# Kernel tuning notes

Hardware: AMD Instinct MI355X
Metric: run time of the kernel (lower is better)

Reference implementation:

```python
import jax, jax.numpy as jnp
import numpy as np

NUM_CONCAT = 3

def setup_inputs() -> dict:
    key = jax.random.key(0)
    k1, k2, k3 = jax.random.split(key, 3)
    x = jax.random.normal(k1, (4, 2048, 4096), dtype=jnp.float32)
    W = jax.random.normal(k2, (12288, 4096), dtype=jnp.float32) * 0.02
    b = jax.random.normal(k3, (12288,), dtype=jnp.float32) * 0.02
    return {"x": x, "W": W, "b": b}

def reference(x, W, b):
    # Fused concat-linear: one GEMM over the concatenated weight, then split.
    # x: [B, S, D]; W: [NUM_CONCAT*H, D]; b: [NUM_CONCAT*H]
    y = jnp.einsum('bsd,od->bso', x, W) + b  # [B, S, NUM_CONCAT*H]
    hidden = y.shape[-1] // NUM_CONCAT
    return tuple(y[..., i * hidden:(i + 1) * hidden] for i in range(NUM_CONCAT))
```

## Files before the change

### kernel.cpp

```cpp
#include <hip/hip_runtime.h>
#include <stdint.h>


typedef __attribute__((ext_vector_type(8))) short short8;
typedef __attribute__((ext_vector_type(4))) float f32x4;

#define BM  256
#define BN  256
#define BKT 64

__device__ __forceinline__ unsigned short f2bf(float f) {
  union { float f; unsigned u; } v; v.f = f;
  unsigned u = v.u;
  u += 0x7FFFu + ((u >> 16) & 1u);
  return (unsigned short)(u >> 16);
}

__global__ void cast_f32_to_bf16(const float* __restrict__ in,
                                 unsigned short* __restrict__ out, int n8) {
  int i = blockIdx.x * blockDim.x + threadIdx.x;
  if (i >= n8) return;
  const float4* p = (const float4*)in;
  float4 a = p[2 * i + 0];
  float4 b = p[2 * i + 1];
  uint4 o;
  o.x = (unsigned)f2bf(a.x) | ((unsigned)f2bf(a.y) << 16);
  o.y = (unsigned)f2bf(a.z) | ((unsigned)f2bf(a.w) << 16);
  o.z = (unsigned)f2bf(b.x) | ((unsigned)f2bf(b.y) << 16);
  o.w = (unsigned)f2bf(b.z) | ((unsigned)f2bf(b.w) << 16);
  ((uint4*)out)[i] = o;
}

__device__ __forceinline__ void gload16(const unsigned short* src, short* dst) {
  __builtin_amdgcn_global_load_lds(
      (const __attribute__((address_space(1))) unsigned int*)src,
      (__attribute__((address_space(3))) unsigned int*)dst, 16, 0, 0);
}

__global__ __launch_bounds__(512, 2)
void gemm256_bias_split(const unsigned short* __restrict__ A,
                        const unsigned short* __restrict__ B,
                        const float* __restrict__ bias,
                        float* __restrict__ out,
                        int M, int N, int K, int H) {
  __shared__ short sA[2][BM * BKT];
  __shared__ short sB[2][BN * BKT];

  const int tid  = threadIdx.x;
  const int lane = tid & 63;
  const int r16  = lane & 15;
  const int q    = lane >> 4;
  const int wave = tid >> 6;
  const int wr   = wave >> 2;
  const int wc   = wave & 3;
  const int AR   = wr * 128;
  const int BR   = wc * 64;

  const int ntx = N / BN;
  int bid = blockIdx.x;
  const int nwg = gridDim.x;
  if ((nwg & 7) == 0) {
    const int cpx = nwg >> 3;
    bid = (bid & 7) * cpx + (bid >> 3);
  }
  const int n0 = (bid % ntx) * BN;
  const int m0 = (bid / ntx) * BM;

  const int NT = K / BKT;

  const int c   = tid & 7;
  const int pr  = tid >> 3;
  const int csz = c ^ (pr & 7);
  const unsigned short* gA = A + (size_t)(m0 + pr) * K + csz * 8;
  const int prB = (pr & 31) + ((tid >> 8) << 6);
  const unsigned short* gB = B + (size_t)(n0 + prB) * K + csz * 8;
  const int dA = pr * 64 + c * 8;
  const int dB = prB * 64 + c * 8;
  const size_t K128 = (size_t)128 * K;

  auto stageA = [&](int buf, int kt, int u) {
    const unsigned short* s = gA + (size_t)(u * 64) * K + kt * BKT;
    short* d = &sA[buf][dA + u * 4096];
    gload16(s, d);
    gload16(s + K128, d + 8192);
  };
  auto stageB = [&](int buf, int kt, int u) {
    const unsigned short* s = gB + (size_t)(u * 32) * K + kt * BKT;
    short* d = &sB[buf][dB + u * 2048];
    gload16(s, d);
    gload16(s + K128, d + 8192);
  };

  const int swz  = r16 & 7;
  const int aoff = (AR + r16) * 64;
  const int boff = (BR + r16) * 64;
  const int ck0  = (q ^ swz) * 8;
  const int ck1  = ((4 + q) ^ swz) * 8;

  f32x4 acc[8][4];
#pragma unroll
  for (int i = 0; i < 8; ++i)
#pragma unroll
    for (int j = 0; j < 4; ++j) acc[i][j] = (f32x4){0.f, 0.f, 0.f, 0.f};

  stageA(0, 0, 0); stageB(0, 0, 0); stageA(0, 0, 1); stageB(0, 0, 1);
  stageA(1, 1, 0); stageB(1, 1, 0); stageA(1, 1, 1);
  asm volatile("s_waitcnt vmcnt(6)" ::: "memory");
  __builtin_amdgcn_s_barrier();

  short8 alo[4][2], ahi[4][2], b01[2][2], b23[2][2];

  for (int j = 0; j < NT; ++j) {
    const int P = j & 1;
    const short* bA = sA[P];
    const short* bB = sB[P];

#pragma unroll
    for (int mf = 0; mf < 4; ++mf) {
      alo[mf][0] = *(const short8*)&bA[aoff + mf * 1024 + ck0];
      alo[mf][1] = *(const short8*)&bA[aoff + mf * 1024 + ck1];
    }
#pragma unroll
    for (int nf = 0; nf < 2; ++nf) {
      b01[nf][0] = *(const short8*)&bB[boff + nf * 1024 + ck0];
      b01[nf][1] = *(const short8*)&bB[boff + nf * 1024 + ck1];
    }
    if (j + 1 < NT) stageB(P ^ 1, j + 1, 1);
    __builtin_amdgcn_s_barrier();
    asm volatile("s_waitcnt lgkmcnt(0)" ::: "memory");
    __builtin_amdgcn_sched_barrier(0);
    __builtin_amdgcn_s_setprio(1);
#pragma unroll
    for (int mf = 0; mf < 4; ++mf)
#pragma unroll
      for (int nf = 0; nf < 2; ++nf) {
        acc[mf][nf] = __builtin_amdgcn_mfma_f32_16x16x32_bf16(alo[mf][0], b01[nf][0], acc[mf][nf], 0, 0, 0);
        acc[mf][nf] = __builtin_amdgcn_mfma_f32_16x16x32_bf16(alo[mf][1], b01[nf][1], acc[mf][nf], 0, 0, 0);
      }
    __builtin_amdgcn_s_setprio(0);
    __builtin_amdgcn_s_barrier();

#pragma unroll
    for (int nf = 0; nf < 2; ++nf) {
      b23[nf][0] = *(const short8*)&bB[boff + (nf + 2) * 1024 + ck0];
      b23[nf][1] = *(const short8*)&bB[boff + (nf + 2) * 1024 + ck1];
    }
    if (j + 2 < NT) stageA(P, j + 2, 0);
    __builtin_amdgcn_s_barrier();
    asm volatile("s_waitcnt lgkmcnt(0)" ::: "memory");
    __builtin_amdgcn_sched_barrier(0);
    __builtin_amdgcn_s_setprio(1);
#pragma unroll
    for (int mf = 0; mf < 4; ++mf)
#pragma unroll
      for (int nf = 0; nf < 2; ++nf) {
        acc[mf][nf + 2] = __builtin_amdgcn_mfma_f32_16x16x32_bf16(alo[mf][0], b23[nf][0], acc[mf][nf + 2], 0, 0, 0);
        acc[mf][nf + 2] = __builtin_amdgcn_mfma_f32_16x16x32_bf16(alo[mf][1], b23[nf][1], acc[mf][nf + 2], 0, 0, 0);
      }
    __builtin_amdgcn_s_setprio(0);
    __builtin_amdgcn_s_barrier();

#pragma unroll
    for (int mf = 0; mf < 4; ++mf) {
      ahi[mf][0] = *(const short8*)&bA[aoff + (mf + 4) * 1024 + ck0];
      ahi[mf][1] = *(const short8*)&bA[aoff + (mf + 4) * 1024 + ck1];
    }
    if (j + 2 < NT) stageB(P, j + 2, 0);
    __builtin_amdgcn_s_barrier();
    asm volatile("s_waitcnt lgkmcnt(0)" ::: "memory");
    __builtin_amdgcn_sched_barrier(0);
    __builtin_amdgcn_s_setprio(1);
#pragma unroll
    for (int mf = 0; mf < 4; ++mf)
#pragma unroll
      for (int nf = 0; nf < 2; ++nf) {
        acc[mf + 4][nf + 2] = __builtin_amdgcn_mfma_f32_16x16x32_bf16(ahi[mf][0], b23[nf][0], acc[mf + 4][nf + 2], 0, 0, 0);
        acc[mf + 4][nf + 2] = __builtin_amdgcn_mfma_f32_16x16x32_bf16(ahi[mf][1], b23[nf][1], acc[mf + 4][nf + 2], 0, 0, 0);
      }
    __builtin_amdgcn_s_setprio(0);
    __builtin_amdgcn_s_barrier();

    if (j + 2 < NT) stageA(P, j + 2, 1);
    __builtin_amdgcn_s_barrier();
    __builtin_amdgcn_s_setprio(1);
#pragma unroll
    for (int mf = 0; mf < 4; ++mf)
#pragma unroll
      for (int nf = 0; nf < 2; ++nf) {
        acc[mf + 4][nf] = __builtin_amdgcn_mfma_f32_16x16x32_bf16(ahi[mf][0], b01[nf][0], acc[mf + 4][nf], 0, 0, 0);
        acc[mf + 4][nf] = __builtin_amdgcn_mfma_f32_16x16x32_bf16(ahi[mf][1], b01[nf][1], acc[mf + 4][nf], 0, 0, 0);
      }
    __builtin_amdgcn_s_setprio(0);
    if (j < NT - 2) asm volatile("s_waitcnt vmcnt(6)" ::: "memory");
    else            asm volatile("s_waitcnt vmcnt(0)" ::: "memory");
    __builtin_amdgcn_s_barrier();
  }

  float bj[4];
#pragma unroll
  for (int nf = 0; nf < 4; ++nf) bj[nf] = bias[n0 + BR + nf * 16 + r16];
  const size_t chunk_elems = (size_t)M * H;
#pragma unroll
  for (int nf = 0; nf < 4; ++nf) {
    const int n  = n0 + BR + nf * 16 + r16;
    const int ci = n / H;
    const int h  = n - ci * H;
    float* obase = out + (size_t)ci * chunk_elems + h;
#pragma unroll
    for (int mf = 0; mf < 8; ++mf) {
      const int mb = m0 + AR + mf * 16 + q * 4;
#pragma unroll
      for (int rr = 0; rr < 4; ++rr) {
        obase[(size_t)(mb + rr) * H] = acc[mf][nf][rr] + bj[nf];
      }
    }
  }
}

#define FTILE 128
#define FBK   64

__global__ __launch_bounds__(256)
void gemm_bias_split_fb(const float* __restrict__ Af32,
                        const float* __restrict__ Bf32,
                        const float* __restrict__ bias,
                        float* __restrict__ out,
                        int M, int N, int K, int H) {
  __shared__ short sA[FTILE * FBK];
  __shared__ short sB[FTILE * FBK];

  const int tid  = threadIdx.x;
  const int lane = tid & 63;
  const int r16  = lane & 15;
  const int q    = lane >> 4;
  const int wave = tid >> 6;
  const int wm   = (wave & 1) * 64;
  const int wn   = (wave >> 1) * 64;
  const int m0   = blockIdx.y * FTILE;
  const int n0   = blockIdx.x * FTILE;

  f32x4 acc[4][4];
#pragma unroll
  for (int i = 0; i < 4; ++i)
#pragma unroll
    for (int j = 0; j < 4; ++j)
      acc[i][j] = (f32x4){0.f, 0.f, 0.f, 0.f};

  for (int k0 = 0; k0 < K; k0 += FBK) {
    __syncthreads();
#pragma unroll
    for (int it = 0; it < 4; ++it) {
      const int chunk = it * 256 + tid;
      const int row   = chunk >> 3;
      const int c     = chunk & 7;
      const int cs    = c ^ (row & 7);
      const float* gA = Af32 + (size_t)(m0 + row) * K + (k0 + cs * 8);
      const float* gB = Bf32 + (size_t)(n0 + row) * K + (k0 + cs * 8);
      float4 a0 = ((const float4*)gA)[0], a1 = ((const float4*)gA)[1];
      float4 b0 = ((const float4*)gB)[0], b1 = ((const float4*)gB)[1];
      short8 va, vb;
      va[0] = (short)f2bf(a0.x); va[1] = (short)f2bf(a0.y);
      va[2] = (short)f2bf(a0.z); va[3] = (short)f2bf(a0.w);
      va[4] = (short)f2bf(a1.x); va[5] = (short)f2bf(a1.y);
      va[6] = (short)f2bf(a1.z); va[7] = (short)f2bf(a1.w);
      vb[0] = (short)f2bf(b0.x); vb[1] = (short)f2bf(b0.y);
      vb[2] = (short)f2bf(b0.z); vb[3] = (short)f2bf(b0.w);
      vb[4] = (short)f2bf(b1.x); vb[5] = (short)f2bf(b1.y);
      vb[6] = (short)f2bf(b1.z); vb[7] = (short)f2bf(b1.w);
      *(short8*)&sA[chunk * 8] = va;
      *(short8*)&sB[chunk * 8] = vb;
    }
    __syncthreads();

#pragma unroll
    for (int ks = 0; ks < 2; ++ks) {
      short8 af[4], bfr[4];
#pragma unroll
      for (int i = 0; i < 4; ++i) {
        const int row = wm + i * 16 + r16;
        const int cc  = ks * 4 + q;
        af[i] = *(const short8*)&sA[row * FBK + (cc ^ (row & 7)) * 8];
      }
#pragma unroll
      for (int j = 0; j < 4; ++j) {
        const int row = wn + j * 16 + r16;
        const int cc  = ks * 4 + q;
        bfr[j] = *(const short8*)&sB[row * FBK + (cc ^ (row & 7)) * 8];
      }
#pragma unroll
      for (int i = 0; i < 4; ++i)
#pragma unroll
        for (int j = 0; j < 4; ++j)
          acc[i][j] = __builtin_amdgcn_mfma_f32_16x16x32_bf16(
              af[i], bfr[j], acc[i][j], 0, 0, 0);
    }
  }

  float bj[4];
#pragma unroll
  for (int j = 0; j < 4; ++j) bj[j] = bias[n0 + wn + j * 16 + r16];
  const size_t chunk_elems = (size_t)M * H;
#pragma unroll
  for (int j = 0; j < 4; ++j) {
    const int n  = n0 + wn + j * 16 + r16;
    const int ci = n / H;
    const int h  = n - ci * H;
    float* obase = out + (size_t)ci * chunk_elems + h;
#pragma unroll
    for (int i = 0; i < 4; ++i) {
      const int mb = m0 + wm + i * 16 + q * 4;
#pragma unroll
      for (int rr = 0; rr < 4; ++rr) {
        obase[(size_t)(mb + rr) * H] = acc[i][j][rr] + bj[j];
      }
    }
  }
}

extern "C" void kernel_launch(void* const* d_in, const int* in_sizes, int n_in,
                              void* d_out, int out_size, void* d_ws, size_t ws_size,
                              hipStream_t stream) {
  const float* x = (const float*)d_in[0];
  const float* W = (const float*)d_in[1];
  const float* b = (const float*)d_in[2];
  float* out = (float*)d_out;

  const int N = in_sizes[2];
  const int K = in_sizes[1] / N;
  const int M = in_sizes[0] / K;
  const int H = N / 3;

  const size_t nA = (size_t)M * K;
  const size_t nB = (size_t)N * K;
  const bool ws_ok = ws_size >= (nA + nB) * sizeof(unsigned short);
  const bool big   = ws_ok && (M % BM == 0) && (N % BN == 0) &&
                     (K % BKT == 0) && (K / BKT >= 4);

  if (big) {
    unsigned short* xa = (unsigned short*)d_ws;
    unsigned short* wb = xa + nA;
    cast_f32_to_bf16<<<(int)((nA / 8 + 255) / 256), 256, 0, stream>>>(x, xa, (int)(nA / 8));
    cast_f32_to_bf16<<<(int)((nB / 8 + 255) / 256), 256, 0, stream>>>(W, wb, (int)(nB / 8));
    const int nblocks = (M / BM) * (N / BN);
    gemm256_bias_split<<<nblocks, 512, 0, stream>>>(xa, wb, b, out, M, N, K, H);
  } else {
    dim3 grid(N / FTILE, M / FTILE);
    gemm_bias_split_fb<<<grid, 256, 0, stream>>>(x, W, b, out, M, N, K, H);
  }
}
```

Before: 1.447 ms.

## Software-pipeline LDS fragment loads across iterations to overlap with MFMA

Restructures the main K-loop so each LDS fragment load is issued one phase ahead of its MFMA use. The next tile's A-low and B01 fragments are prefetched during the last phase of the current iteration. Full lgkmcnt(0) waits become partial waits so LDS reads overlap with matrix math, and several barriers are removed. The cost is more register pressure and tighter reasoning about waitcnt and barrier ordering, which could expose LDS read/write races between buffers.

```diff
diff --git a/kernel.cpp b/kernel.cpp
--- a/kernel.cpp
+++ b/kernel.cpp
@@ -110,23 +110,64 @@
 
   short8 alo[4][2], ahi[4][2], b01[2][2], b23[2][2];
 
+#pragma unroll
+  for (int mf = 0; mf < 4; ++mf) {
+    alo[mf][0] = *(const short8*)&sA[0][aoff + mf * 1024 + ck0];
+    alo[mf][1] = *(const short8*)&sA[0][aoff + mf * 1024 + ck1];
+  }
+#pragma unroll
+  for (int nf = 0; nf < 2; ++nf) {
+    b01[nf][0] = *(const short8*)&sB[0][boff + nf * 1024 + ck0];
+    b01[nf][1] = *(const short8*)&sB[0][boff + nf * 1024 + ck1];
+  }
+
   for (int j = 0; j < NT; ++j) {
     const int P = j & 1;
-    const short* bA = sA[P];
-    const short* bB = sB[P];
-
+    const short* bA  = sA[P];
+    const short* bB  = sB[P];
+    const short* bA1 = sA[P ^ 1];
+    const short* bB1 = sB[P ^ 1];
+
+    __builtin_amdgcn_s_barrier();
+    if (j + 1 < NT) stageB(P ^ 1, j + 1, 1);
+#pragma unroll
+    for (int nf = 0; nf < 2; ++nf) {
+      b23[nf][0] = *(const short8*)&bB[boff + (nf + 2) * 1024 + ck0];
+      b23[nf][1] = *(const short8*)&bB[boff + (nf + 2) * 1024 + ck1];
+    }
+    asm volatile("s_waitcnt lgkmcnt(4)" ::: "memory");
+    __builtin_amdgcn_sched_barrier(0);
+    __builtin_amdgcn_s_setprio(1);
+#pragma unroll
+    for (int mf = 0; mf < 4; ++mf)
+#pragma unroll
+      for (int nf = 0; nf < 2; ++nf) {
+        acc[mf][nf] = __builtin_amdgcn_mfma_f32_16x16x32_bf16(alo[mf][0], b01[nf][0], acc[mf][nf], 0, 0, 0);
+        acc[mf][nf] = __builtin_amdgcn_mfma_f32_16x16x32_bf16(alo[mf][1], b01[nf][1], acc[mf][nf], 0, 0, 0);
+      }
+    __builtin_amdgcn_s_setprio(0);
+
+    __builtin_amdgcn_s_barrier();
+    if (j + 2 < NT) stageA(P, j + 2, 0);
 #pragma unroll
     for (int mf = 0; mf < 4; ++mf) {
-      alo[mf][0] = *(const short8*)&bA[aoff + mf * 1024 + ck0];
-      alo[mf][1] = *(const short8*)&bA[aoff + mf * 1024 + ck1];
-    }
-#pragma unroll
-    for (int nf = 0; nf < 2; ++nf) {
-      b01[nf][0] = *(const short8*)&bB[boff + nf * 1024 + ck0];
-      b01[nf][1] = *(const short8*)&bB[boff + nf * 1024 + ck1];
-    }
-    if (j + 1 < NT) stageB(P ^ 1, j + 1, 1);
+      ahi[mf][0] = *(const short8*)&bA[aoff + (mf + 4) * 1024 + ck0];
+      ahi[mf][1] = *(const short8*)&bA[aoff + (mf + 4) * 1024 + ck1];
+    }
+    asm volatile("s_waitcnt lgkmcnt(8)" ::: "memory");
+    __builtin_amdgcn_sched_barrier(0);
+    __builtin_amdgcn_s_setprio(1);
+#pragma unroll
+    for (int mf = 0; mf < 4; ++mf)
+#pragma unroll
+      for (int nf = 0; nf < 2; ++nf) {
+        acc[mf][nf + 2] = __builtin_amdgcn_mfma_f32_16x16x32_bf16(alo[mf][0], b23[nf][0], acc[mf][nf + 2], 0, 0, 0);
+        acc[mf][nf + 2] = __builtin_amdgcn_mfma_f32_16x16x32_bf16(alo[mf][1], b23[nf][1], acc[mf][nf + 2], 0, 0, 0);
+      }
+    __builtin_amdgcn_s_setprio(0);
+
     __builtin_amdgcn_s_barrier();
+    if (j + 2 < NT) stageB(P, j + 2, 0);
     asm volatile("s_waitcnt lgkmcnt(0)" ::: "memory");
     __builtin_amdgcn_sched_barrier(0);
     __builtin_amdgcn_s_setprio(1);
@@ -134,66 +175,41 @@
     for (int mf = 0; mf < 4; ++mf)
 #pragma unroll
       for (int nf = 0; nf < 2; ++nf) {
-        acc[mf][nf] = __builtin_amdgcn_mfma_f32_16x16x32_bf16(alo[mf][0], b01[nf][0], acc[mf][nf], 0, 0, 0);
-        acc[mf][nf] = __builtin_amdgcn_mfma_f32_16x16x32_bf16(alo[mf][1], b01[nf][1], acc[mf][nf], 0, 0, 0);
-      }
-    __builtin_amdgcn_s_setprio(0);
-    __builtin_amdgcn_s_barrier();
-
-#pragma unroll
-    for (int nf = 0; nf < 2; ++nf) {
-      b23[nf][0] = *(const short8*)&bB[boff + (nf + 2) * 1024 + ck0];
-      b23[nf][1] = *(const short8*)&bB[boff + (nf + 2) * 1024 + ck1];
-    }
-    if (j + 2 < NT) stageA(P, j + 2, 0);
-    __builtin_amdgcn_s_barrier();
-    asm volatile("s_waitcnt lgkmcnt(0)" ::: "memory");
-    __builtin_amdgcn_sched_barrier(0);
-    __builtin_amdgcn_s_setprio(1);
-#pragma unroll
-    for (int mf = 0; mf < 4; ++mf)
-#pragma unroll
-      for (int nf = 0; nf < 2; ++nf) {
-        acc[mf][nf + 2] = __builtin_amdgcn_mfma_f32_16x16x32_bf16(alo[mf][0], b23[nf][0], acc[mf][nf + 2], 0, 0, 0);
-        acc[mf][nf + 2] = __builtin_amdgcn_mfma_f32_16x16x32_bf16(alo[mf][1], b23[nf][1], acc[mf][nf + 2], 0, 0, 0);
-      }
-    __builtin_amdgcn_s_setprio(0);
-    __builtin_amdgcn_s_barrier();
-
-#pragma unroll
-    for (int mf = 0; mf < 4; ++mf) {
-      ahi[mf][0] = *(const short8*)&bA[aoff + (mf + 4) * 1024 + ck0];
-      ahi[mf][1] = *(const short8*)&bA[aoff + (mf + 4) * 1024 + ck1];
-    }
-    if (j + 2 < NT) stageB(P, j + 2, 0);
-    __builtin_amdgcn_s_barrier();
-    asm volatile("s_waitcnt lgkmcnt(0)" ::: "memory");
-    __builtin_amdgcn_sched_barrier(0);
-    __builtin_amdgcn_s_setprio(1);
-#pragma unroll
-    for (int mf = 0; mf < 4; ++mf)
-#pragma unroll
-      for (int nf = 0; nf < 2; ++nf) {
         acc[mf + 4][nf + 2] = __builtin_amdgcn_mfma_f32_16x16x32_bf16(ahi[mf][0], b23[nf][0], acc[mf + 4][nf + 2], 0, 0, 0);
         acc[mf + 4][nf + 2] = __builtin_amdgcn_mfma_f32_16x16x32_bf16(ahi[mf][1], b23[nf][1], acc[mf + 4][nf + 2], 0, 0, 0);
-      }
-    __builtin_amdgcn_s_setprio(0);
-    __builtin_amdgcn_s_barrier();
-
-    if (j + 2 < NT) stageA(P, j + 2, 1);
-    __builtin_amdgcn_s_barrier();
-    __builtin_amdgcn_s_setprio(1);
-#pragma unroll
-    for (int mf = 0; mf < 4; ++mf)
-#pragma unroll
-      for (int nf = 0; nf < 2; ++nf) {
-        acc[mf + 4][nf] = __builtin_amdgcn_mfma_f32_16x16x32_bf16(ahi[mf][0], b01[nf][0], acc[mf + 4][nf], 0, 0, 0);
-        acc[mf + 4][nf] = __builtin_amdgcn_mfma_f32_16x16x32_bf16(ahi[mf][1], b01[nf][1], acc[mf + 4][nf], 0, 0, 0);
       }
     __builtin_amdgcn_s_setprio(0);
     if (j < NT - 2) asm volatile("s_waitcnt vmcnt(6)" ::: "memory");
     else            asm volatile("s_waitcnt vmcnt(0)" ::: "memory");
+
     __builtin_amdgcn_s_barrier();
+    if (j + 2 < NT) stageA(P, j + 2, 1);
+    if (j + 1 < NT) {
+#pragma unroll
+      for (int mf = 0; mf < 4; ++mf) {
+        alo[mf][0] = *(const short8*)&bA1[aoff + mf * 1024 + ck0];
+        alo[mf][1] = *(const short8*)&bA1[aoff + mf * 1024 + ck1];
+      }
+    }
+    __builtin_amdgcn_sched_barrier(0);
+    __builtin_amdgcn_s_setprio(1);
+#pragma unroll
+    for (int mf = 0; mf < 4; ++mf)
+#pragma unroll
+      for (int nf = 0; nf < 2; ++nf) {
+        acc[mf + 4][nf] = __builtin_amdgcn_mfma_f32_16x16x32_bf16(ahi[mf][0], b01[nf][0], acc[mf + 4][nf], 0, 0, 0);
+        acc[mf + 4][nf] = __builtin_amdgcn_mfma_f32_16x16x32_bf16(ahi[mf][1], b01[nf][1], acc[mf + 4][nf], 0, 0, 0);
+      }
+    __builtin_amdgcn_s_setprio(0);
+    if (j + 1 < NT) {
+#pragma unroll
+      for (int nf = 0; nf < 2; ++nf) {
+        b01[nf][0] = *(const short8*)&bB1[boff + nf * 1024 + ck0];
+        b01[nf][1] = *(const short8*)&bB1[boff + nf * 1024 + ck1];
+      }
+    }
+    if (j < NT - 2) asm volatile("s_waitcnt vmcnt(4)" ::: "memory");
+    else            asm volatile("s_waitcnt vmcnt(0)" ::: "memory");
   }
 
   float bj[4];
```

Result: slower. 1.743 ms (+20.5%).

## Split LDS fragment loads with partial lgkmcnt waits and fuse cast kernels

Applied to the files above, without the earlier changes.

Reorders each GEMM sub-phase so the global-to-LDS stage is issued before the LDS register loads. The loads are split into halves with partial s_waitcnt lgkmcnt waits, so MFMAs on the first half can start while the second half is still arriving. The two fp32-to-bf16 cast launches are also merged into one kernel to save a launch. The partial waits depend on exact counts of outstanding LDS operations, so the compiler emitting those instructions in a different order could introduce races.

```diff
diff --git a/kernel.cpp b/kernel.cpp
--- a/kernel.cpp
+++ b/kernel.cpp
@@ -16,19 +16,27 @@
   return (unsigned short)(u >> 16);
 }
 
-__global__ void cast_f32_to_bf16(const float* __restrict__ in,
-                                 unsigned short* __restrict__ out, int n8) {
-  int i = blockIdx.x * blockDim.x + threadIdx.x;
-  if (i >= n8) return;
+__global__ void cast2_f32_to_bf16(const float* __restrict__ inA,
+                                  unsigned short* __restrict__ outA, long long nA8,
+                                  const float* __restrict__ inB,
+                                  unsigned short* __restrict__ outB, long long nB8) {
+  long long i = (long long)blockIdx.x * blockDim.x + threadIdx.x;
+  const float* in; unsigned short* out; long long k;
+  if (i < nA8) { in = inA; out = outA; k = i; }
+  else {
+    k = i - nA8;
+    if (k >= nB8) return;
+    in = inB; out = outB;
+  }
   const float4* p = (const float4*)in;
-  float4 a = p[2 * i + 0];
-  float4 b = p[2 * i + 1];
+  float4 a = p[2 * k + 0];
+  float4 b = p[2 * k + 1];
   uint4 o;
   o.x = (unsigned)f2bf(a.x) | ((unsigned)f2bf(a.y) << 16);
   o.y = (unsigned)f2bf(a.z) | ((unsigned)f2bf(a.w) << 16);
   o.z = (unsigned)f2bf(b.x) | ((unsigned)f2bf(b.y) << 16);
   o.w = (unsigned)f2bf(b.z) | ((unsigned)f2bf(b.w) << 16);
-  ((uint4*)out)[i] = o;
+  ((uint4*)out)[k] = o;
 }
 
 __device__ __forceinline__ void gload16(const unsigned short* src, short* dst) {
@@ -115,63 +123,99 @@
     const short* bA = sA[P];
     const short* bB = sB[P];
 
-#pragma unroll
-    for (int mf = 0; mf < 4; ++mf) {
-      alo[mf][0] = *(const short8*)&bA[aoff + mf * 1024 + ck0];
-      alo[mf][1] = *(const short8*)&bA[aoff + mf * 1024 + ck1];
-    }
+    if (j + 1 < NT) stageB(P ^ 1, j + 1, 1);
 #pragma unroll
     for (int nf = 0; nf < 2; ++nf) {
       b01[nf][0] = *(const short8*)&bB[boff + nf * 1024 + ck0];
       b01[nf][1] = *(const short8*)&bB[boff + nf * 1024 + ck1];
     }
-    if (j + 1 < NT) stageB(P ^ 1, j + 1, 1);
-    __builtin_amdgcn_s_barrier();
-    asm volatile("s_waitcnt lgkmcnt(0)" ::: "memory");
+#pragma unroll
+    for (int mf = 0; mf < 2; ++mf) {
+      alo[mf][0] = *(const short8*)&bA[aoff + mf * 1024 + ck0];
+      alo[mf][1] = *(const short8*)&bA[aoff + mf * 1024 + ck1];
+    }
+    __builtin_amdgcn_sched_barrier(0);
+#pragma unroll
+    for (int mf = 2; mf < 4; ++mf) {
+      alo[mf][0] = *(const short8*)&bA[aoff + mf * 1024 + ck0];
+      alo[mf][1] = *(const short8*)&bA[aoff + mf * 1024 + ck1];
+    }
+    asm volatile("s_waitcnt lgkmcnt(8)" ::: "memory");
+    __builtin_amdgcn_s_barrier();
+    asm volatile("s_waitcnt lgkmcnt(4)" ::: "memory");
     __builtin_amdgcn_sched_barrier(0);
     __builtin_amdgcn_s_setprio(1);
 #pragma unroll
-    for (int mf = 0; mf < 4; ++mf)
+    for (int mf = 0; mf < 2; ++mf)
 #pragma unroll
       for (int nf = 0; nf < 2; ++nf) {
         acc[mf][nf] = __builtin_amdgcn_mfma_f32_16x16x32_bf16(alo[mf][0], b01[nf][0], acc[mf][nf], 0, 0, 0);
         acc[mf][nf] = __builtin_amdgcn_mfma_f32_16x16x32_bf16(alo[mf][1], b01[nf][1], acc[mf][nf], 0, 0, 0);
       }
+    asm volatile("s_waitcnt lgkmcnt(0)" ::: "memory");
+    __builtin_amdgcn_sched_barrier(0);
+#pragma unroll
+    for (int mf = 2; mf < 4; ++mf)
+#pragma unroll
+      for (int nf = 0; nf < 2; ++nf) {
+        acc[mf][nf] = __builtin_amdgcn_mfma_f32_16x16x32_bf16(alo[mf][0], b01[nf][0], acc[mf][nf], 0, 0, 0);
+        acc[mf][nf] = __builtin_amdgcn_mfma_f32_16x16x32_bf16(alo[mf][1], b01[nf][1], acc[mf][nf], 0, 0, 0);
+      }
     __builtin_amdgcn_s_setprio(0);
     __builtin_amdgcn_s_barrier();
 
-#pragma unroll
-    for (int nf = 0; nf < 2; ++nf) {
-      b23[nf][0] = *(const short8*)&bB[boff + (nf + 2) * 1024 + ck0];
-      b23[nf][1] = *(const short8*)&bB[boff + (nf + 2) * 1024 + ck1];
-    }
     if (j + 2 < NT) stageA(P, j + 2, 0);
-    __builtin_amdgcn_s_barrier();
+    b23[0][0] = *(const short8*)&bB[boff + 2 * 1024 + ck0];
+    b23[0][1] = *(const short8*)&bB[boff + 2 * 1024 + ck1];
+    __builtin_amdgcn_sched_barrier(0);
+    b23[1][0] = *(const short8*)&bB[boff + 3 * 1024 + ck0];
+    b23[1][1] = *(const short8*)&bB[boff + 3 * 1024 + ck1];
+    __builtin_amdgcn_s_barrier();
+    asm volatile("s_waitcnt lgkmcnt(2)" ::: "memory");
+    __builtin_amdgcn_sched_barrier(0);
+    __builtin_amdgcn_s_setprio(1);
+#pragma unroll
+    for (int mf = 0; mf < 4; ++mf) {
+      acc[mf][2] = __builtin_amdgcn_mfma_f32_16x16x32_bf16(alo[mf][0], b23[0][0], acc[mf][2], 0, 0, 0);
+      acc[mf][2] = __builtin_amdgcn_mfma_f32_16x16x32_bf16(alo[mf][1], b23[0][1], acc[mf][2], 0, 0, 0);
+    }
     asm volatile("s_waitcnt lgkmcnt(0)" ::: "memory");
     __builtin_amdgcn_sched_barrier(0);
-    __builtin_amdgcn_s_setprio(1);
-#pragma unroll
-    for (int mf = 0; mf < 4; ++mf)
-#pragma unroll
-      for (int nf = 0; nf < 2; ++nf) {
-        acc[mf][nf + 2] = __builtin_amdgcn_mfma_f32_16x16x32_bf16(alo[mf][0], b23[nf][0], acc[mf][nf + 2], 0, 0, 0);
-        acc[mf][nf + 2] = __builtin_amdgcn_mfma_f32_16x16x32_bf16(alo[mf][1], b23[nf][1], acc[mf][nf + 2], 0, 0, 0);
-      }
+#pragma unroll
+    for (int mf = 0; mf < 4; ++mf) {
+      acc[mf][3] = __builtin_amdgcn_mfma_f32_16x16x32_bf16(alo[mf][0], b23[1][0], acc[mf][3], 0, 0, 0);
+      acc[mf][3] = __builtin_amdgcn_mfma_f32_16x16x32_bf16(alo[mf][1], b23[1][1], acc[mf][3], 0, 0, 0);
+    }
     __builtin_amdgcn_s_setprio(0);
     __builtin_amdgcn_s_barrier();
 
-#pragma unroll
-    for (int mf = 0; mf < 4; ++mf) {
+    if (j + 2 < NT) stageB(P, j + 2, 0);
+#pragma unroll
+    for (int mf = 0; mf < 2; ++mf) {
       ahi[mf][0] = *(const short8*)&bA[aoff + (mf + 4) * 1024 + ck0];
       ahi[mf][1] = *(const short8*)&bA[aoff + (mf + 4) * 1024 + ck1];
     }
-    if (j + 2 < NT) stageB(P, j + 2, 0);
-    __builtin_amdgcn_s_barrier();
+    __builtin_amdgcn_sched_barrier(0);
+#pragma unroll
+    for (int mf = 2; mf < 4; ++mf) {
+      ahi[mf][0] = *(const short8*)&bA[aoff + (mf + 4) * 1024 + ck0];
+      ahi[mf][1] = *(const short8*)&bA[aoff + (mf + 4) * 1024 + ck1];
+    }
+    __builtin_amdgcn_s_barrier();
+    asm volatile("s_waitcnt lgkmcnt(4)" ::: "memory");
+    __builtin_amdgcn_sched_barrier(0);
+    __builtin_amdgcn_s_setprio(1);
+#pragma unroll
+    for (int mf = 0; mf < 2; ++mf)
+#pragma unroll
+      for (int nf = 0; nf < 2; ++nf) {
+        acc[mf + 4][nf + 2] = __builtin_amdgcn_mfma_f32_16x16x32_bf16(ahi[mf][0], b23[nf][0], acc[mf + 4][nf + 2], 0, 0, 0);
+        acc[mf + 4][nf + 2] = __builtin_amdgcn_mfma_f32_16x16x32_bf16(ahi[mf][1], b23[nf][1], acc[mf + 4][nf + 2], 0, 0, 0);
+      }
     asm volatile("s_waitcnt lgkmcnt(0)" ::: "memory");
     __builtin_amdgcn_sched_barrier(0);
-    __builtin_amdgcn_s_setprio(1);
-#pragma unroll
-    for (int mf = 0; mf < 4; ++mf)
+#pragma unroll
+    for (int mf = 2; mf < 4; ++mf)
 #pragma unroll
       for (int nf = 0; nf < 2; ++nf) {
         acc[mf + 4][nf + 2] = __builtin_amdgcn_mfma_f32_16x16x32_bf16(ahi[mf][0], b23[nf][0], acc[mf + 4][nf + 2], 0, 0, 0);
@@ -339,8 +383,11 @@
   if (big) {
     unsigned short* xa = (unsigned short*)d_ws;
     unsigned short* wb = xa + nA;
-    cast_f32_to_bf16<<<(int)((nA / 8 + 255) / 256), 256, 0, stream>>>(x, xa, (int)(nA / 8));
-    cast_f32_to_bf16<<<(int)((nB / 8 + 255) / 256), 256, 0, stream>>>(W, wb, (int)(nB / 8));
+    const long long nA8 = (long long)(nA / 8);
+    const long long nB8 = (long long)(nB / 8);
+    const long long tot = nA8 + nB8;
+    cast2_f32_to_bf16<<<(int)((tot + 255) / 256), 256, 0, stream>>>(
+        x, xa, nA8, W, wb, nB8);
     const int nblocks = (M / BM) * (N / BN);
     gemm256_bias_split<<<nblocks, 512, 0, stream>>>(xa, wb, b, out, M, N, K, H);
   } else {
```

Result: slower. 1.566 ms (+8.2%).
